# Optimization experiments

Hardware: AMD Instinct MI355X
Metric: run time of the kernel (lower is better)

The kernel has to match this reference:

```python
import jax, jax.numpy as jnp
import numpy as np

N_NODES = 100000
N_GRAPHS = 512
NEG_SLOPE = 0.2
EPS = 1e-16


def gat_conv(x, W, a_src, a_dst, bias, src, dst, heads, out_ch, concat):
    # x: [N, Fin]; W: [Fin, heads*out_ch]; a_src/a_dst: [heads, out_ch]
    N = x.shape[0]
    h = (x @ W).reshape(N, heads, out_ch)                      # [N,H,C]
    alpha_src = jnp.einsum('nhc,hc->nh', h, a_src)             # [N,H]
    alpha_dst = jnp.einsum('nhc,hc->nh', h, a_dst)             # [N,H]
    e = alpha_src[src] + alpha_dst[dst]                        # [E,H]
    e = jnp.where(e > 0, e, NEG_SLOPE * e)                     # leaky relu
    # segment softmax over incoming edges per destination node
    m = jax.ops.segment_max(e, dst, num_segments=N)            # [N,H]
    m = jnp.where(jnp.isfinite(m), m, 0.0)
    ee = jnp.exp(e - m[dst])
    denom = jax.ops.segment_sum(ee, dst, num_segments=N)       # [N,H]
    alpha = ee / (denom[dst] + EPS)                            # [E,H]
    msg = h[src] * alpha[:, :, None]                           # [E,H,C]
    out = jax.ops.segment_sum(msg, dst, num_segments=N)        # [N,H,C]
    if concat:
        out = out.reshape(N, heads * out_ch)
    else:
        out = out.mean(axis=1)
    return out + bias


def setup_inputs() -> dict:
    key = jax.random.key(0)
    ks = jax.random.split(key, 12)
    x = jax.random.normal(ks[0], (N_NODES, 128), dtype=jnp.float32)
    edge_index = jax.random.randint(ks[1], (2, 1600000), 0, N_NODES, dtype=jnp.int64)
    batch = jnp.sort(jax.random.randint(ks[2], (N_NODES,), 0, N_GRAPHS, dtype=jnp.int64))
    s = 0.1
    W1 = jax.random.normal(ks[3], (128, 64), dtype=jnp.float32) * s
    a_src1 = jax.random.normal(ks[4], (8, 8), dtype=jnp.float32) * s
    a_dst1 = jax.random.normal(ks[5], (8, 8), dtype=jnp.float32) * s
    b1 = jnp.zeros((64,), dtype=jnp.float32)
    W2 = jax.random.normal(ks[6], (64, 10), dtype=jnp.float32) * s
    a_src2 = jax.random.normal(ks[7], (1, 10), dtype=jnp.float32) * s
    a_dst2 = jax.random.normal(ks[8], (1, 10), dtype=jnp.float32) * s
    b2 = jnp.zeros((10,), dtype=jnp.float32)
    return {"x": x, "edge_index": edge_index, "batch": batch,
            "W1": W1, "a_src1": a_src1, "a_dst1": a_dst1, "b1": b1,
            "W2": W2, "a_src2": a_src2, "a_dst2": a_dst2, "b2": b2}


def reference(x, edge_index, batch, W1, a_src1, a_dst1, b1, W2, a_src2, a_dst2, b2):
    N = x.shape[0]
    # PyG GATConv default add_self_loops=True
    loops = jnp.arange(N, dtype=edge_index.dtype)
    src = jnp.concatenate([edge_index[0], loops])
    dst = jnp.concatenate([edge_index[1], loops])
    # eval mode: dropout layers are identity
    h = gat_conv(x, W1, a_src1, a_dst1, b1, src, dst, heads=8, out_ch=8, concat=True)
    h = jax.nn.elu(h)
    h = gat_conv(h, W2, a_src2, a_dst2, b2, src, dst, heads=1, out_ch=10, concat=False)
    # global mean pool over graphs
    sums = jax.ops.segment_sum(h, batch, num_segments=N_GRAPHS)        # [G,10]
    cnts = jax.ops.segment_sum(jnp.ones((N, 1), h.dtype), batch, num_segments=N_GRAPHS)
    pooled = sums / jnp.maximum(cnts, 1.0)
    return jax.nn.log_softmax(pooled, axis=1)
```

## Files before the change

kernel.cpp:

```cpp
#include <hip/hip_runtime.h>
#include <math.h>

#define L2E 1.44269504088896f
#define LRELU(v) fmaxf((v), 0.2f * (v))

__device__ __forceinline__ float fexp2(float v) { return __builtin_amdgcn_exp2f(v); }

__device__ __forceinline__ unsigned short f2bf(float f) {
    unsigned u = __float_as_uint(f);
    u += 0x7FFFu + ((u >> 16) & 1u);
    return (unsigned short)(u >> 16);
}
__device__ __forceinline__ float bf2f(unsigned short b) {
    return __uint_as_float((unsigned)b << 16);
}

typedef __attribute__((ext_vector_type(8))) short bf16x8;
typedef __attribute__((ext_vector_type(4))) float f32x4;

#define UPD4(mm, dd, AA, ev, GG)           \
    {                                      \
        float mn_ = fmaxf(mm, ev);         \
        float sc_ = fexp2(mm - mn_);       \
        float w_  = fexp2(ev - mn_);       \
        dd = dd * sc_ + w_;                \
        AA.x = AA.x * sc_ + w_ * (GG).x;   \
        AA.y = AA.y * sc_ + w_ * (GG).y;   \
        AA.z = AA.z * sc_ + w_ * (GG).z;   \
        AA.w = AA.w * sc_ + w_ * (GG).w;   \
        mm = mn_;                          \
    }
#define UPD1(mm, dd, aa, ev, hv)           \
    {                                      \
        float mn_ = fmaxf(mm, ev);         \
        float sc_ = fexp2(mm - mn_);       \
        float w_  = fexp2(ev - mn_);       \
        dd = dd * sc_ + w_;                \
        aa = aa * sc_ + w_ * (hv);         \
        mm = mn_;                          \
    }

#define CH 4096

__device__ __forceinline__ float4 b4f(ushort4 u) {
    float4 r;
    r.x = bf2f(u.x); r.y = bf2f(u.y); r.z = bf2f(u.z); r.w = bf2f(u.w);
    return r;
}

__global__ __launch_bounds__(256) void k_gemm1_mfma(
        const float* __restrict__ x, const float* __restrict__ W,
        unsigned short* __restrict__ h1b, int N, int ntiles) {
    int tid = threadIdx.x;
    int w = tid >> 6, l = tid & 63;
    int c0 = w * 16;
    int lr = l & 15;
    int lg = l >> 4;

    bf16x8 bfr[4];
#pragma unroll
    for (int kk = 0; kk < 4; ++kk)
#pragma unroll
        for (int j = 0; j < 8; ++j)
            bfr[kk][j] = (short)f2bf(W[(size_t)(kk * 32 + lg * 8 + j) * 64 + c0 + lr]);

    for (int t = blockIdx.x; t < ntiles; t += gridDim.x) {
        int n0 = t * 16;
        int n = n0 + lr;
        const float4* xr = (const float4*)(x + (size_t)(n < N ? n : 0) * 128);
        f32x4 acc = {0.f, 0.f, 0.f, 0.f};
#pragma unroll
        for (int kk = 0; kk < 4; ++kk) {
            float4 u0 = xr[kk * 8 + lg * 2];
            float4 u1 = xr[kk * 8 + lg * 2 + 1];
            bf16x8 afr;
            afr[0] = (short)f2bf(u0.x); afr[1] = (short)f2bf(u0.y);
            afr[2] = (short)f2bf(u0.z); afr[3] = (short)f2bf(u0.w);
            afr[4] = (short)f2bf(u1.x); afr[5] = (short)f2bf(u1.y);
            afr[6] = (short)f2bf(u1.z); afr[7] = (short)f2bf(u1.w);
            acc = __builtin_amdgcn_mfma_f32_16x16x32_bf16(afr, bfr[kk], acc, 0, 0, 0);
        }
#pragma unroll
        for (int r = 0; r < 4; ++r) {
            int nn = n0 + lg * 4 + r;
            if (nn < N) h1b[(size_t)nn * 64 + c0 + lr] = f2bf(acc[r]);
        }
    }
}

__global__ void k_alpha(const unsigned short* __restrict__ h1b,
                        const float* __restrict__ a_src, const float* __restrict__ a_dst,
                        unsigned short* __restrict__ asrcb, float* __restrict__ adst, int N) {
    int t = blockIdx.x * 256 + threadIdx.x;
    if (t >= N * 8) return;
    int n = t >> 3, h = t & 7;
    uint4 hw = *(const uint4*)&h1b[(size_t)n * 64 + h * 8];
    const unsigned short* hu = (const unsigned short*)&hw;
    const float* as = a_src + h * 8;
    const float* ad = a_dst + h * 8;
    float s = 0.f, d = 0.f;
#pragma unroll
    for (int c = 0; c < 8; ++c) {
        float hv = bf2f(hu[c]);
        s = fmaf(hv, as[c], s);
        d = fmaf(hv, ad[c], d);
    }
    asrcb[t] = f2bf(s * L2E);
    adst[t] = d * L2E;
}


__global__ __launch_bounds__(256) void k_bhist(const int* __restrict__ dstE,
                                               const int* __restrict__ batch,
                                               int E, int NB, int G, int* __restrict__ bh) {
    __shared__ int lh[512];
    int tid = threadIdx.x, b = blockIdx.x;
    lh[tid] = 0; lh[tid + 256] = 0;
    __syncthreads();
#pragma unroll
    for (int i = 0; i < CH / 256; ++i) {
        int e = b * CH + i * 256 + tid;
        if (e < E) atomicAdd(&lh[batch[dstE[e]]], 1);
    }
    __syncthreads();
    if (tid < G)       bh[(size_t)tid * NB + b] = lh[tid];
    if (tid + 256 < G) bh[(size_t)(tid + 256) * NB + b] = lh[tid + 256];
}

__global__ __launch_bounds__(512) void k_mscan(const int* __restrict__ bh, int NB,
                                               int* __restrict__ pstart, int* __restrict__ total) {
    __shared__ int buf[512];
    int bin = blockIdx.x, t = threadIdx.x;
    int v = (t < NB) ? bh[(size_t)bin * NB + t] : 0;
    buf[t] = v;
    __syncthreads();
    for (int off = 1; off < 512; off <<= 1) {
        int u = (t >= off) ? buf[t - off] : 0;
        __syncthreads();
        buf[t] += u;
        __syncthreads();
    }
    if (t < NB) pstart[(size_t)bin * NB + t] = buf[t] - v;
    if (t == 511) total[bin] = buf[511];
}

__global__ __launch_bounds__(1024) void k_scan_top(const int* __restrict__ total, int nb,
                                                   int* __restrict__ boff) {
    __shared__ int buf[1024];
    int t = threadIdx.x;
    int v = (t < nb) ? total[t] : 0;
    buf[t] = v;
    __syncthreads();
    for (int off = 1; off < 1024; off <<= 1) {
        int u = (t >= off) ? buf[t - off] : 0;
        __syncthreads();
        buf[t] += u;
        __syncthreads();
    }
    if (t < nb) boff[t] = buf[t] - v;
}

__global__ __launch_bounds__(256) void k_bscatter(const int* __restrict__ srcE,
                                                  const int* __restrict__ dstE,
                                                  const int* __restrict__ batch,
                                                  const int* __restrict__ boff,
                                                  const int* __restrict__ pstart,
                                                  int E, int NB, int G, int2* __restrict__ pairs) {
    __shared__ int lstart[512];
    __shared__ int lc[512];
    int tid = threadIdx.x, b = blockIdx.x;
#pragma unroll
    for (int j = tid; j < 512; j += 256) {
        lstart[j] = (j < G) ? boff[j] + pstart[(size_t)j * NB + b] : 0;
        lc[j] = 0;
    }
    __syncthreads();
#pragma unroll
    for (int i = 0; i < CH / 256; ++i) {
        int e = b * CH + i * 256 + tid;
        if (e < E) {
            int s = srcE[e], d = dstE[e];
            int bin = batch[d];
            int old = atomicAdd(&lc[bin], 1);
            pairs[lstart[bin] + old] = make_int2(s, d);
        }
    }
}

__global__ __launch_bounds__(512) void k_csr_local(const int2* __restrict__ pairs,
                                                   const int* __restrict__ boff,
                                                   const int* __restrict__ batch,
                                                   int E, int N, int G,
                                                   int* __restrict__ cnt, int* __restrict__ excl,
                                                   int* __restrict__ srcs) {
    __shared__ int lcnt[512];
    __shared__ int buf[512];
    __shared__ int lcur[512];
    int g = blockIdx.x, t = threadIdx.x;
    int lo = 0, hi = N;
    while (lo < hi) { int mid = (lo + hi) >> 1; if (batch[mid] < g) lo = mid + 1; else hi = mid; }
    int ns = lo;
    hi = N;
    while (lo < hi) { int mid = (lo + hi) >> 1; if (batch[mid] < g + 1) lo = mid + 1; else hi = mid; }
    int ne = lo;
    int lnodes = ne - ns;
    int es = boff[g];
    int ee = (g + 1 < G) ? boff[g + 1] : E;

    lcnt[t] = 0;
    __syncthreads();
    for (int e = es + t; e < ee; e += 512) atomicAdd(&lcnt[pairs[e].y - ns], 1);
    __syncthreads();
    int v = lcnt[t];
    buf[t] = v;
    __syncthreads();
    for (int off = 1; off < 512; off <<= 1) {
        int u = (t >= off) ? buf[t - off] : 0;
        __syncthreads();
        buf[t] += u;
        __syncthreads();
    }
    int lex = buf[t] - v;
    lcur[t] = lex;
    if (t < lnodes) {
        cnt[ns + t] = v;
        excl[ns + t] = es + lex;
    }
    __syncthreads();
    for (int e = es + t; e < ee; e += 512) {
        int2 p = pairs[e];
        int pos = atomicAdd(&lcur[p.y - ns], 1);
        srcs[es + pos] = p.x;
    }
}

__global__ void k_gather1(const int* __restrict__ srcs, const int* __restrict__ excl,
                          const int* __restrict__ cnt,
                          const unsigned short* __restrict__ asrcb, const float* __restrict__ adst1,
                          const unsigned short* __restrict__ h1b, float* __restrict__ agg, int N) {
    int tid = blockIdx.x * 256 + threadIdx.x;
    int wave = tid >> 6;
    int lane = threadIdx.x & 63;
    int q = lane >> 4;
    int l = lane & 15;
    int wid = wave * 4 + q;
    if (wid >= N) return;
    int h = l >> 1;
    int c0 = l * 4;

    int beg = excl[wid];
    int cw  = cnt[wid];
    const int* sp = srcs + beg;
    float adh = adst1[wid * 8 + h];

    float4 A0 = b4f(*(const ushort4*)&h1b[(size_t)wid * 64 + c0]);
    float m0 = LRELU(bf2f(asrcb[wid * 8 + h]) + adh), d0 = 1.f;
    float4 A1 = {0.f, 0.f, 0.f, 0.f}, A2 = A1, A3 = A1;
    float m1 = -INFINITY, d1 = 0.f;
    float m2 = -INFINITY, d2 = 0.f;
    float m3 = -INFINITY, d3 = 0.f;

    int i = 0;
    for (; i + 4 <= cw; i += 4) {
        int s0 = sp[i], s1 = sp[i + 1], s2 = sp[i + 2], s3 = sp[i + 3];
        float e0 = LRELU(bf2f(asrcb[s0 * 8 + h]) + adh);
        float e1 = LRELU(bf2f(asrcb[s1 * 8 + h]) + adh);
        float e2 = LRELU(bf2f(asrcb[s2 * 8 + h]) + adh);
        float e3 = LRELU(bf2f(asrcb[s3 * 8 + h]) + adh);
        float4 g0 = b4f(*(const ushort4*)&h1b[(size_t)s0 * 64 + c0]);
        float4 g1 = b4f(*(const ushort4*)&h1b[(size_t)s1 * 64 + c0]);
        float4 g2 = b4f(*(const ushort4*)&h1b[(size_t)s2 * 64 + c0]);
        float4 g3 = b4f(*(const ushort4*)&h1b[(size_t)s3 * 64 + c0]);
        UPD4(m0, d0, A0, e0, g0);
        UPD4(m1, d1, A1, e1, g1);
        UPD4(m2, d2, A2, e2, g2);
        UPD4(m3, d3, A3, e3, g3);
    }
    for (; i < cw; ++i) {
        int s = sp[i];
        float ev = LRELU(bf2f(asrcb[s * 8 + h]) + adh);
        float4 gv = b4f(*(const ushort4*)&h1b[(size_t)s * 64 + c0]);
        UPD4(m0, d0, A0, ev, gv);
    }
    float mM = fmaxf(fmaxf(m0, m1), fmaxf(m2, m3));
    float w0 = fexp2(m0 - mM), w1 = fexp2(m1 - mM);
    float w2 = fexp2(m2 - mM), w3 = fexp2(m3 - mM);
    float den = d0 * w0 + d1 * w1 + d2 * w2 + d3 * w3;
    float inv = 1.f / (den + 1e-16f);
    float4 r;
    r.x = (A0.x * w0 + A1.x * w1 + A2.x * w2 + A3.x * w3) * inv;
    r.y = (A0.y * w0 + A1.y * w1 + A2.y * w2 + A3.y * w3) * inv;
    r.z = (A0.z * w0 + A1.z * w1 + A2.z * w2 + A3.z * w3) * inv;
    r.w = (A0.w * w0 + A1.w * w1 + A2.w * w2 + A3.w * w3) * inv;
    *(float4*)&agg[(size_t)wid * 64 + c0] = r;
}

__global__ void k_fin1(const float* __restrict__ agg, const float* __restrict__ b1,
                       const float* __restrict__ W2,
                       const float* __restrict__ a_src2, const float* __restrict__ a_dst2,
                       unsigned short* __restrict__ h2b, unsigned short* __restrict__ asrc2b,
                       float* __restrict__ adst2, int N) {
    int n = blockIdx.x * 256 + threadIdx.x;
    if (n >= N) return;
    float acc[10];
#pragma unroll
    for (int j = 0; j < 10; ++j) acc[j] = 0.f;
    const float* ar = agg + (size_t)n * 64;
#pragma unroll 8
    for (int k = 0; k < 64; ++k) {
        float r = ar[k] + b1[k];
        r = r > 0.f ? r : expm1f(r);
#pragma unroll
        for (int j = 0; j < 10; ++j) acc[j] = fmaf(r, W2[k * 10 + j], acc[j]);
    }
    float s = 0.f, d = 0.f;
    unsigned pw[5];
#pragma unroll
    for (int j = 0; j < 10; j += 2) {
        s = fmaf(acc[j], a_src2[j], s);     d = fmaf(acc[j], a_dst2[j], d);
        s = fmaf(acc[j+1], a_src2[j+1], s); d = fmaf(acc[j+1], a_dst2[j+1], d);
        pw[j >> 1] = (unsigned)f2bf(acc[j]) | ((unsigned)f2bf(acc[j+1]) << 16);
    }
    unsigned* hw = (unsigned*)&h2b[(size_t)n * 10];
#pragma unroll
    for (int j = 0; j < 5; ++j) hw[j] = pw[j];
    asrc2b[n] = f2bf(s * L2E);
    adst2[n] = d * L2E;
}

__global__ void k_gather2(const int* __restrict__ srcs, const int* __restrict__ excl,
                          const int* __restrict__ cnt,
                          const unsigned short* __restrict__ asrc2b, const float* __restrict__ adst2,
                          const unsigned short* __restrict__ h2b, float* __restrict__ agg2, int N) {
    int tid = blockIdx.x * 256 + threadIdx.x;
    int wave = tid >> 6;
    int lane = threadIdx.x & 63;
    int q = lane >> 4;
    int l = lane & 15;
    int wid = wave * 4 + q;
    if (wid >= N) return;

    int beg = excl[wid];
    int cw  = cnt[wid];
    const int* sp = srcs + beg;
    float adn = adst2[wid];
    bool ld = l < 10;

    float m0 = LRELU(bf2f(asrc2b[wid]) + adn), d0 = 1.f;
    float a0 = ld ? bf2f(h2b[(size_t)wid * 10 + l]) : 0.f;
    float m1 = -INFINITY, d1 = 0.f, a1 = 0.f;
    float m2 = -INFINITY, d2 = 0.f, a2 = 0.f;
    float m3 = -INFINITY, d3 = 0.f, a3 = 0.f;

    int i = 0;
    for (; i + 4 <= cw; i += 4) {
        int s0 = sp[i], s1 = sp[i + 1], s2 = sp[i + 2], s3 = sp[i + 3];
        float e0 = LRELU(bf2f(asrc2b[s0]) + adn);
        float e1 = LRELU(bf2f(asrc2b[s1]) + adn);
        float e2 = LRELU(bf2f(asrc2b[s2]) + adn);
        float e3 = LRELU(bf2f(asrc2b[s3]) + adn);
        float g0 = ld ? bf2f(h2b[(size_t)s0 * 10 + l]) : 0.f;
        float g1 = ld ? bf2f(h2b[(size_t)s1 * 10 + l]) : 0.f;
        float g2 = ld ? bf2f(h2b[(size_t)s2 * 10 + l]) : 0.f;
        float g3 = ld ? bf2f(h2b[(size_t)s3 * 10 + l]) : 0.f;
        UPD1(m0, d0, a0, e0, g0);
        UPD1(m1, d1, a1, e1, g1);
        UPD1(m2, d2, a2, e2, g2);
        UPD1(m3, d3, a3, e3, g3);
    }
    for (; i < cw; ++i) {
        int s = sp[i];
        float ev = LRELU(bf2f(asrc2b[s]) + adn);
        float gv = ld ? bf2f(h2b[(size_t)s * 10 + l]) : 0.f;
        UPD1(m0, d0, a0, ev, gv);
    }
    float mM = fmaxf(fmaxf(m0, m1), fmaxf(m2, m3));
    float w0 = fexp2(m0 - mM), w1 = fexp2(m1 - mM);
    float w2 = fexp2(m2 - mM), w3 = fexp2(m3 - mM);
    float den = d0 * w0 + d1 * w1 + d2 * w2 + d3 * w3;
    float acc = a0 * w0 + a1 * w1 + a2 * w2 + a3 * w3;
    if (ld) agg2[(size_t)wid * 10 + l] = acc / (den + 1e-16f);
}

__global__ void k_pool_final(const float* __restrict__ agg2, const float* __restrict__ b2,
                             const int* __restrict__ batch, float* __restrict__ out,
                             int N, int G) {
    int g = blockIdx.x;
    int lo = 0, hi = N;
    while (lo < hi) { int mid = (lo + hi) >> 1; if (batch[mid] < g) lo = mid + 1; else hi = mid; }
    int s = lo;
    lo = s; hi = N;
    while (lo < hi) { int mid = (lo + hi) >> 1; if (batch[mid] < g + 1) lo = mid + 1; else hi = mid; }
    int e = lo;
    int tid = threadIdx.x;
    float acc[10];
#pragma unroll
    for (int j = 0; j < 10; ++j) acc[j] = 0.f;
    for (int n = s + tid; n < e; n += 256) {
        const float* r = agg2 + (size_t)n * 10;
#pragma unroll
        for (int j = 0; j < 10; ++j) acc[j] += r[j];
    }
    __shared__ float red[256 * 10];
#pragma unroll
    for (int j = 0; j < 10; ++j) red[tid * 10 + j] = acc[j];
    __syncthreads();
    for (int st = 128; st > 0; st >>= 1) {
        if (tid < st)
#pragma unroll
            for (int j = 0; j < 10; ++j) red[tid * 10 + j] += red[(tid + st) * 10 + j];
        __syncthreads();
    }
    if (tid == 0) {
        int c = e - s;
        float v[10], m = -1e30f;
#pragma unroll
        for (int j = 0; j < 10; ++j) {
            v[j] = (c > 0) ? red[j] / (float)c + b2[j] : 0.f;
            m = fmaxf(m, v[j]);
        }
        float ssum = 0.f;
#pragma unroll
        for (int j = 0; j < 10; ++j) ssum += expf(v[j] - m);
        float ls = logf(ssum);
#pragma unroll
        for (int j = 0; j < 10; ++j) out[(size_t)g * 10 + j] = v[j] - m - ls;
    }
}

extern "C" void kernel_launch(void* const* d_in, const int* in_sizes, int n_in,
                              void* d_out, int out_size, void* d_ws, size_t ws_size,
                              hipStream_t stream) {
    const float* x     = (const float*)d_in[0];
    const int*   ei    = (const int*)d_in[1];
    const int*   batch = (const int*)d_in[2];
    const float* W1    = (const float*)d_in[3];
    const float* as1w  = (const float*)d_in[4];
    const float* ad1w  = (const float*)d_in[5];
    const float* b1    = (const float*)d_in[6];
    const float* W2    = (const float*)d_in[7];
    const float* as2w  = (const float*)d_in[8];
    const float* ad2w  = (const float*)d_in[9];
    const float* b2    = (const float*)d_in[10];

    const int N  = in_sizes[0] / 128;
    const int E  = in_sizes[1] / 2;
    const int G  = out_size / 10;
    const int* srcE = ei;
    const int* dstE = ei + E;

    auto cdiv = [](long long a, long long b) { return (int)((a + b - 1) / b); };
    const int NB = cdiv(E, CH);

    size_t Nz = (size_t)N;
    unsigned short* h1b = (unsigned short*)d_ws;
    float* agg2  = (float*)d_ws;
    unsigned short* asrc1b = h1b + Nz * 64;
    float* adst1 = (float*)(asrc1b + Nz * 8);
    unsigned short* h2b = (unsigned short*)(adst1 + Nz * 8);
    unsigned short* asrc2b = h2b + Nz * 10;
    float* adst2 = (float*)(asrc2b + Nz + (Nz & 1));
    float* agg1  = adst2 + Nz;
    int2*  pairs = (int2*)agg1;
    int* cntA    = (int*)(agg1 + Nz * 64);
    int* exclA   = cntA + Nz;
    int* srcsA   = exclA + Nz;
    int* bhA     = srcsA + E;
    int* pstartA = bhA + (size_t)512 * NB;
    int* totalA  = pstartA + (size_t)512 * NB;
    int* boffA   = totalA + 512;

    const int B = 256;

    int ntiles = cdiv(N, 16);
    int gB = ntiles < 2048 ? ntiles : 2048;
    k_gemm1_mfma<<<gB, B, 0, stream>>>(x, W1, h1b, N, ntiles);
    k_alpha<<<cdiv((long long)N * 8, B), B, 0, stream>>>(h1b, as1w, ad1w, asrc1b, adst1, N);

    k_bhist<<<NB, B, 0, stream>>>(dstE, batch, E, NB, G, bhA);
    k_mscan<<<512, 512, 0, stream>>>(bhA, NB, pstartA, totalA);
    k_scan_top<<<1, 1024, 0, stream>>>(totalA, G, boffA);
    k_bscatter<<<NB, B, 0, stream>>>(srcE, dstE, batch, boffA, pstartA, E, NB, G, pairs);
    k_csr_local<<<G, 512, 0, stream>>>(pairs, boffA, batch, E, N, G, cntA, exclA, srcsA);

    k_gather1<<<cdiv(N, 16), B, 0, stream>>>(srcsA, exclA, cntA, asrc1b, adst1, h1b, agg1, N);
    k_fin1<<<cdiv(N, B), B, 0, stream>>>(agg1, b1, W2, as2w, ad2w, h2b, asrc2b, adst2, N);

    k_gather2<<<cdiv(N, 16), B, 0, stream>>>(srcsA, exclA, cntA, asrc2b, adst2, h2b, agg2, N);

    k_pool_final<<<G, B, 0, stream>>>(agg2, b2, batch, (float*)d_out, N, G);
}
```

Measured before the change: 207.6 us.

## Fuse histogram into GEMM launch, widen gather1 lanes, vectorize fin1 loads

The batch histogram now runs as extra blocks of the GEMM kernel, so one launch disappears and the two independent jobs can overlap. In gather1, each lane now handles a full head (8 channels, one 16-byte load per edge) instead of half a head, so a wave covers 8 destination nodes rather than 4. Fewer lanes repeat the per-edge attention-logit load and exp computation, at the cost of more registers per thread. fin1 reads agg and bias as float4 vectors instead of scalars.

```diff
diff --git a/kernel.cpp b/kernel.cpp
--- a/kernel.cpp
+++ b/kernel.cpp
@@ -18,17 +18,21 @@
 typedef __attribute__((ext_vector_type(8))) short bf16x8;
 typedef __attribute__((ext_vector_type(4))) float f32x4;
 
-#define UPD4(mm, dd, AA, ev, GG)           \
-    {                                      \
-        float mn_ = fmaxf(mm, ev);         \
-        float sc_ = fexp2(mm - mn_);       \
-        float w_  = fexp2(ev - mn_);       \
-        dd = dd * sc_ + w_;                \
-        AA.x = AA.x * sc_ + w_ * (GG).x;   \
-        AA.y = AA.y * sc_ + w_ * (GG).y;   \
-        AA.z = AA.z * sc_ + w_ * (GG).z;   \
-        AA.w = AA.w * sc_ + w_ * (GG).w;   \
-        mm = mn_;                          \
+#define UPD8(mm, dd, Aa, Ab, ev, U)                                       \
+    {                                                                     \
+        float mn_ = fmaxf(mm, ev);                                        \
+        float sc_ = fexp2(mm - mn_);                                      \
+        float w_  = fexp2(ev - mn_);                                      \
+        dd = dd * sc_ + w_;                                               \
+        Aa.x = Aa.x * sc_ + w_ * __uint_as_float((U).x << 16);            \
+        Aa.y = Aa.y * sc_ + w_ * __uint_as_float((U).x & 0xffff0000u);    \
+        Aa.z = Aa.z * sc_ + w_ * __uint_as_float((U).y << 16);            \
+        Aa.w = Aa.w * sc_ + w_ * __uint_as_float((U).y & 0xffff0000u);    \
+        Ab.x = Ab.x * sc_ + w_ * __uint_as_float((U).z << 16);            \
+        Ab.y = Ab.y * sc_ + w_ * __uint_as_float((U).z & 0xffff0000u);    \
+        Ab.z = Ab.z * sc_ + w_ * __uint_as_float((U).w << 16);            \
+        Ab.w = Ab.w * sc_ + w_ * __uint_as_float((U).w & 0xffff0000u);    \
+        mm = mn_;                                                         \
     }
 #define UPD1(mm, dd, aa, ev, hv)           \
     {                                      \
@@ -42,15 +46,26 @@
 
 #define CH 4096
 
-__device__ __forceinline__ float4 b4f(ushort4 u) {
-    float4 r;
-    r.x = bf2f(u.x); r.y = bf2f(u.y); r.z = bf2f(u.z); r.w = bf2f(u.w);
-    return r;
-}
-
-__global__ __launch_bounds__(256) void k_gemm1_mfma(
+__global__ __launch_bounds__(256) void k_gemm1_hist(
         const float* __restrict__ x, const float* __restrict__ W,
-        unsigned short* __restrict__ h1b, int N, int ntiles) {
+        unsigned short* __restrict__ h1b, int N, int ntiles, int gemmBlocks,
+        const int* __restrict__ dstE, const int* __restrict__ batch,
+        int E, int NB, int G, int* __restrict__ bh) {
+    __shared__ int lh[512];
+    if ((int)blockIdx.x >= gemmBlocks) {
+        int tid = threadIdx.x, b = blockIdx.x - gemmBlocks;
+        lh[tid] = 0; lh[tid + 256] = 0;
+        __syncthreads();
+#pragma unroll
+        for (int i = 0; i < CH / 256; ++i) {
+            int e = b * CH + i * 256 + tid;
+            if (e < E) atomicAdd(&lh[batch[dstE[e]]], 1);
+        }
+        __syncthreads();
+        if (tid < G)       bh[(size_t)tid * NB + b] = lh[tid];
+        if (tid + 256 < G) bh[(size_t)(tid + 256) * NB + b] = lh[tid + 256];
+        return;
+    }
     int tid = threadIdx.x;
     int w = tid >> 6, l = tid & 63;
     int c0 = w * 16;
@@ -64,7 +79,7 @@
         for (int j = 0; j < 8; ++j)
             bfr[kk][j] = (short)f2bf(W[(size_t)(kk * 32 + lg * 8 + j) * 64 + c0 + lr]);
 
-    for (int t = blockIdx.x; t < ntiles; t += gridDim.x) {
+    for (int t = blockIdx.x; t < ntiles; t += gemmBlocks) {
         int n0 = t * 16;
         int n = n0 + lr;
         const float4* xr = (const float4*)(x + (size_t)(n < N ? n : 0) * 128);
@@ -109,23 +124,6 @@
     adst[t] = d * L2E;
 }
 
-
-__global__ __launch_bounds__(256) void k_bhist(const int* __restrict__ dstE,
-                                               const int* __restrict__ batch,
-                                               int E, int NB, int G, int* __restrict__ bh) {
-    __shared__ int lh[512];
-    int tid = threadIdx.x, b = blockIdx.x;
-    lh[tid] = 0; lh[tid + 256] = 0;
-    __syncthreads();
-#pragma unroll
-    for (int i = 0; i < CH / 256; ++i) {
-        int e = b * CH + i * 256 + tid;
-        if (e < E) atomicAdd(&lh[batch[dstE[e]]], 1);
-    }
-    __syncthreads();
-    if (tid < G)       bh[(size_t)tid * NB + b] = lh[tid];
-    if (tid + 256 < G) bh[(size_t)(tid + 256) * NB + b] = lh[tid + 256];
-}
 
 __global__ __launch_bounds__(512) void k_mscan(const int* __restrict__ bh, int NB,
                                                int* __restrict__ pstart, int* __restrict__ total) {
@@ -241,21 +239,26 @@
     int tid = blockIdx.x * 256 + threadIdx.x;
     int wave = tid >> 6;
     int lane = threadIdx.x & 63;
-    int q = lane >> 4;
-    int l = lane & 15;
-    int wid = wave * 4 + q;
+    int q = lane >> 3;
+    int l = lane & 7;
+    int wid = wave * 8 + q;
     if (wid >= N) return;
-    int h = l >> 1;
-    int c0 = l * 4;
+    int c0 = l * 8;
 
     int beg = excl[wid];
     int cw  = cnt[wid];
     const int* sp = srcs + beg;
-    float adh = adst1[wid * 8 + h];
-
-    float4 A0 = b4f(*(const ushort4*)&h1b[(size_t)wid * 64 + c0]);
-    float m0 = LRELU(bf2f(asrcb[wid * 8 + h]) + adh), d0 = 1.f;
-    float4 A1 = {0.f, 0.f, 0.f, 0.f}, A2 = A1, A3 = A1;
+    float adh = adst1[wid * 8 + l];
+
+    uint4 us = *(const uint4*)&h1b[(size_t)wid * 64 + c0];
+    float4 A0a, A0b;
+    A0a.x = __uint_as_float(us.x << 16); A0a.y = __uint_as_float(us.x & 0xffff0000u);
+    A0a.z = __uint_as_float(us.y << 16); A0a.w = __uint_as_float(us.y & 0xffff0000u);
+    A0b.x = __uint_as_float(us.z << 16); A0b.y = __uint_as_float(us.z & 0xffff0000u);
+    A0b.z = __uint_as_float(us.w << 16); A0b.w = __uint_as_float(us.w & 0xffff0000u);
+    float m0 = LRELU(bf2f(asrcb[wid * 8 + l]) + adh), d0 = 1.f;
+    float4 Z = {0.f, 0.f, 0.f, 0.f};
+    float4 A1a = Z, A1b = Z, A2a = Z, A2b = Z, A3a = Z, A3b = Z;
     float m1 = -INFINITY, d1 = 0.f;
     float m2 = -INFINITY, d2 = 0.f;
     float m3 = -INFINITY, d3 = 0.f;
@@ -263,36 +266,41 @@
     int i = 0;
     for (; i + 4 <= cw; i += 4) {
         int s0 = sp[i], s1 = sp[i + 1], s2 = sp[i + 2], s3 = sp[i + 3];
-        float e0 = LRELU(bf2f(asrcb[s0 * 8 + h]) + adh);
-        float e1 = LRELU(bf2f(asrcb[s1 * 8 + h]) + adh);
-        float e2 = LRELU(bf2f(asrcb[s2 * 8 + h]) + adh);
-        float e3 = LRELU(bf2f(asrcb[s3 * 8 + h]) + adh);
-        float4 g0 = b4f(*(const ushort4*)&h1b[(size_t)s0 * 64 + c0]);
-        float4 g1 = b4f(*(const ushort4*)&h1b[(size_t)s1 * 64 + c0]);
-        float4 g2 = b4f(*(const ushort4*)&h1b[(size_t)s2 * 64 + c0]);
-        float4 g3 = b4f(*(const ushort4*)&h1b[(size_t)s3 * 64 + c0]);
-        UPD4(m0, d0, A0, e0, g0);
-        UPD4(m1, d1, A1, e1, g1);
-        UPD4(m2, d2, A2, e2, g2);
-        UPD4(m3, d3, A3, e3, g3);
+        float e0 = LRELU(bf2f(asrcb[s0 * 8 + l]) + adh);
+        float e1 = LRELU(bf2f(asrcb[s1 * 8 + l]) + adh);
+        float e2 = LRELU(bf2f(asrcb[s2 * 8 + l]) + adh);
+        float e3 = LRELU(bf2f(asrcb[s3 * 8 + l]) + adh);
+        uint4 u0 = *(const uint4*)&h1b[(size_t)s0 * 64 + c0];
+        uint4 u1 = *(const uint4*)&h1b[(size_t)s1 * 64 + c0];
+        uint4 u2 = *(const uint4*)&h1b[(size_t)s2 * 64 + c0];
+        uint4 u3 = *(const uint4*)&h1b[(size_t)s3 * 64 + c0];
+        UPD8(m0, d0, A0a, A0b, e0, u0);
+        UPD8(m1, d1, A1a, A1b, e1, u1);
+        UPD8(m2, d2, A2a, A2b, e2, u2);
+        UPD8(m3, d3, A3a, A3b, e3, u3);
     }
     for (; i < cw; ++i) {
         int s = sp[i];
-        float ev = LRELU(bf2f(asrcb[s * 8 + h]) + adh);
-        float4 gv = b4f(*(const ushort4*)&h1b[(size_t)s * 64 + c0]);
-        UPD4(m0, d0, A0, ev, gv);
+        float ev = LRELU(bf2f(asrcb[s * 8 + l]) + adh);
+        uint4 uv = *(const uint4*)&h1b[(size_t)s * 64 + c0];
+        UPD8(m0, d0, A0a, A0b, ev, uv);
     }
     float mM = fmaxf(fmaxf(m0, m1), fmaxf(m2, m3));
     float w0 = fexp2(m0 - mM), w1 = fexp2(m1 - mM);
     float w2 = fexp2(m2 - mM), w3 = fexp2(m3 - mM);
     float den = d0 * w0 + d1 * w1 + d2 * w2 + d3 * w3;
     float inv = 1.f / (den + 1e-16f);
-    float4 r;
-    r.x = (A0.x * w0 + A1.x * w1 + A2.x * w2 + A3.x * w3) * inv;
-    r.y = (A0.y * w0 + A1.y * w1 + A2.y * w2 + A3.y * w3) * inv;
-    r.z = (A0.z * w0 + A1.z * w1 + A2.z * w2 + A3.z * w3) * inv;
-    r.w = (A0.w * w0 + A1.w * w1 + A2.w * w2 + A3.w * w3) * inv;
-    *(float4*)&agg[(size_t)wid * 64 + c0] = r;
+    float4 Ra, Rb;
+    Ra.x = (A0a.x * w0 + A1a.x * w1 + A2a.x * w2 + A3a.x * w3) * inv;
+    Ra.y = (A0a.y * w0 + A1a.y * w1 + A2a.y * w2 + A3a.y * w3) * inv;
+    Ra.z = (A0a.z * w0 + A1a.z * w1 + A2a.z * w2 + A3a.z * w3) * inv;
+    Ra.w = (A0a.w * w0 + A1a.w * w1 + A2a.w * w2 + A3a.w * w3) * inv;
+    Rb.x = (A0b.x * w0 + A1b.x * w1 + A2b.x * w2 + A3b.x * w3) * inv;
+    Rb.y = (A0b.y * w0 + A1b.y * w1 + A2b.y * w2 + A3b.y * w3) * inv;
+    Rb.z = (A0b.z * w0 + A1b.z * w1 + A2b.z * w2 + A3b.z * w3) * inv;
+    Rb.w = (A0b.w * w0 + A1b.w * w1 + A2b.w * w2 + A3b.w * w3) * inv;
+    *(float4*)&agg[(size_t)wid * 64 + c0] = Ra;
+    *(float4*)&agg[(size_t)wid * 64 + c0 + 4] = Rb;
 }
 
 __global__ void k_fin1(const float* __restrict__ agg, const float* __restrict__ b1,
@@ -305,13 +313,22 @@
     float acc[10];
 #pragma unroll
     for (int j = 0; j < 10; ++j) acc[j] = 0.f;
-    const float* ar = agg + (size_t)n * 64;
-#pragma unroll 8
-    for (int k = 0; k < 64; ++k) {
-        float r = ar[k] + b1[k];
-        r = r > 0.f ? r : expm1f(r);
-#pragma unroll
-        for (int j = 0; j < 10; ++j) acc[j] = fmaf(r, W2[k * 10 + j], acc[j]);
+    const float4* ar4 = (const float4*)(agg + (size_t)n * 64);
+    const float4* b14 = (const float4*)b1;
+#pragma unroll 4
+    for (int kq = 0; kq < 16; ++kq) {
+        float4 a4 = ar4[kq];
+        float4 bq = b14[kq];
+        float r[4];
+        r[0] = a4.x + bq.x; r[1] = a4.y + bq.y;
+        r[2] = a4.z + bq.z; r[3] = a4.w + bq.w;
+#pragma unroll
+        for (int t = 0; t < 4; ++t) {
+            float rv = r[t] > 0.f ? r[t] : expm1f(r[t]);
+            const float* wr = W2 + (kq * 4 + t) * 10;
+#pragma unroll
+            for (int j = 0; j < 10; ++j) acc[j] = fmaf(rv, wr[j], acc[j]);
+        }
     }
     float s = 0.f, d = 0.f;
     unsigned pw[5];
@@ -474,16 +491,16 @@
 
     int ntiles = cdiv(N, 16);
     int gB = ntiles < 2048 ? ntiles : 2048;
-    k_gemm1_mfma<<<gB, B, 0, stream>>>(x, W1, h1b, N, ntiles);
+    k_gemm1_hist<<<gB + NB, B, 0, stream>>>(x, W1, h1b, N, ntiles, gB,
+                                            dstE, batch, E, NB, G, bhA);
     k_alpha<<<cdiv((long long)N * 8, B), B, 0, stream>>>(h1b, as1w, ad1w, asrc1b, adst1, N);
 
-    k_bhist<<<NB, B, 0, stream>>>(dstE, batch, E, NB, G, bhA);
     k_mscan<<<512, 512, 0, stream>>>(bhA, NB, pstartA, totalA);
     k_scan_top<<<1, 1024, 0, stream>>>(totalA, G, boffA);
     k_bscatter<<<NB, B, 0, stream>>>(srcE, dstE, batch, boffA, pstartA, E, NB, G, pairs);
     k_csr_local<<<G, 512, 0, stream>>>(pairs, boffA, batch, E, N, G, cntA, exclA, srcsA);
 
-    k_gather1<<<cdiv(N, 16), B, 0, stream>>>(srcsA, exclA, cntA, asrc1b, adst1, h1b, agg1, N);
+    k_gather1<<<cdiv(N, 32), B, 0, stream>>>(srcsA, exclA, cntA, asrc1b, adst1, h1b, agg1, N);
     k_fin1<<<cdiv(N, B), B, 0, stream>>>(agg1, b1, W2, as2w, ad2w, h2b, asrc2b, adst2, N);
 
     k_gather2<<<cdiv(N, 16), B, 0, stream>>>(srcsA, exclA, cntA, asrc2b, adst2, h2b, agg2, N);
```

Result: faster. 199.5 us (-3.9%).
